# Performance work log

Measured on AMD Instinct MI355X. Metric: run time of the kernel, lower is better.

The kernel has to match this reference:

```python
import jax, jax.numpy as jnp
import numpy as np

HEAD_DIM = 64
N_HEADS = 32
N_KV_HEADS = 8
ROPE_THETA = 10000.0


def _rotate_half(x):
    h = x.shape[-1] // 2
    return jnp.concatenate([-x[..., h:], x[..., :h]], axis=-1)


def _rope_cos_sin(position_ids, head_dim, theta, dtype):
    # position_ids: [b, s] int
    inv_freq = 1.0 / (theta ** (jnp.arange(0, head_dim, 2, dtype=jnp.float32) / head_dim))
    freqs = position_ids.astype(jnp.float32)[..., None] * inv_freq  # [b, s, hd/2]
    emb = jnp.concatenate([freqs, freqs], axis=-1)                  # [b, s, hd]
    return jnp.cos(emb).astype(dtype), jnp.sin(emb).astype(dtype)


def setup_inputs() -> dict:
    key = jax.random.key(0)
    ks = jax.random.split(key, 5)
    B, S, H = 2, 2048, 2048
    KVD = N_KV_HEADS * HEAD_DIM
    x = jax.random.normal(ks[0], (B, S, H), dtype=jnp.float32)
    position_ids = jnp.broadcast_to(jnp.arange(S, dtype=jnp.int64), (B, S))
    # additive causal mask: 0 on/below diagonal, -1e9 above
    causal = jnp.triu(jnp.full((S, S), -1e9, dtype=jnp.float32), k=1)
    mask = causal[None, None, :, :]
    sc = 1.0 / np.sqrt(H)
    wq = jax.random.normal(ks[1], (H, H), dtype=jnp.float32) * sc
    wk = jax.random.normal(ks[2], (KVD, H), dtype=jnp.float32) * sc
    wv = jax.random.normal(ks[3], (KVD, H), dtype=jnp.float32) * sc
    wo = jax.random.normal(ks[4], (H, H), dtype=jnp.float32) * sc
    return {"x": x, "position_ids": position_ids, "mask": mask,
            "wq": wq, "wk": wk, "wv": wv, "wo": wo}


def reference(x, position_ids, mask, wq, wk, wv, wo):
    b, s, h = x.shape
    kv_groups = N_HEADS // N_KV_HEADS
    # projections (Linear with weight [out, in])
    xq = jnp.einsum('bsh,oh->bso', x, wq)
    xk = jnp.einsum('bsh,oh->bso', x, wk)
    xv = jnp.einsum('bsh,oh->bso', x, wv)
    q = xq.reshape(b, s, N_HEADS, HEAD_DIM).transpose(0, 2, 1, 3)      # [b,H,s,d]
    k = xk.reshape(b, s, N_KV_HEADS, HEAD_DIM).transpose(0, 2, 1, 3)   # [b,Hk,s,d]
    v = xv.reshape(b, s, N_KV_HEADS, HEAD_DIM).transpose(0, 2, 1, 3)
    cos, sin = _rope_cos_sin(position_ids, HEAD_DIM, ROPE_THETA, x.dtype)
    cos = cos[:, None, :, :]  # [b,1,s,d]
    sin = sin[:, None, :, :]
    q = q * cos + _rotate_half(q) * sin
    k = k * cos + _rotate_half(k) * sin
    # GQA expand
    k = jnp.repeat(k, kv_groups, axis=1)  # [b,H,s,d]
    v = jnp.repeat(v, kv_groups, axis=1)
    scale = 1.0 / np.sqrt(HEAD_DIM)
    attn = jnp.einsum('bhqd,bhkd->bhqk', q, k) * scale
    attn = attn + mask[:, :, :s, :s]
    attn = jax.nn.softmax(attn.astype(jnp.float32), axis=-1).astype(q.dtype)
    out = jnp.einsum('bhqk,bhkd->bhqd', attn, v)        # [b,H,s,d]
    out = out.transpose(0, 2, 1, 3).reshape(b, s, h)
    return jnp.einsum('bsh,oh->bso', out, wo)
```

## Files before the change

kernel.cpp:

```cpp
#include <hip/hip_runtime.h>

typedef __bf16 bf16;
typedef __bf16 bf16x4 __attribute__((ext_vector_type(4)));
typedef __bf16 bf16x8 __attribute__((ext_vector_type(8)));
typedef float f32x4 __attribute__((ext_vector_type(4)));

#define MFMA16(a, b, c) __builtin_amdgcn_mfma_f32_16x16x32_bf16(a, b, c, 0, 0, 0)
#define L2E 1.44269504088896340736f

__device__ inline float exp2_hw(float x) {
  float r;
  asm("v_exp_f32 %0, %1" : "=v"(r) : "v"(x));
  return r;
}

__device__ inline bf16x8 cvt8(const float* __restrict__ p) {
  float4 f0 = ((const float4*)p)[0];
  float4 f1 = ((const float4*)p)[1];
  bf16x8 v;
  v[0] = (bf16)f0.x; v[1] = (bf16)f0.y; v[2] = (bf16)f0.z; v[3] = (bf16)f0.w;
  v[4] = (bf16)f1.x; v[5] = (bf16)f1.y; v[6] = (bf16)f1.z; v[7] = (bf16)f1.w;
  return v;
}

__device__ inline void gl_lds16(const bf16* g, bf16* l) {
  __builtin_amdgcn_global_load_lds(
      (const __attribute__((address_space(1))) unsigned int*)g,
      (__attribute__((address_space(3))) unsigned int*)l, 16, 0, 0);
}

__global__ void detect_kernel(const unsigned* __restrict__ mask,
                              int* __restrict__ flag) {
  *flag = (mask[0] != 0u) ? 1 : 0;
}

__global__ __launch_bounds__(256) void convert_kernel(
    const void* __restrict__ s0, bf16* __restrict__ d0, int n0,
    const void* __restrict__ s1, bf16* __restrict__ d1, int n1,
    const void* __restrict__ s2, bf16* __restrict__ d2, int n2,
    const void* __restrict__ s3, bf16* __restrict__ d3, int n3,
    float2* __restrict__ tab, const int* __restrict__ flag) {
  const int gid = blockIdx.x * 256 + threadIdx.x;
  if (tab && gid < 65536) {
    int s = gid >> 5, fi = gid & 31;
    float inv = 1.0f / powf(10000.0f, (float)(2 * fi) / 64.0f);
    float fr = (float)s * inv;
    tab[gid] = make_float2(cosf(fr), sinf(fr));
  }
  const int isb = *flag;
  const int c0 = n0 >> 3, c1 = c0 + (n1 >> 3), c2 = c1 + (n2 >> 3);
  const int total = c2 + (n3 >> 3);
  for (int c = gid; c < total; c += gridDim.x * 256) {
    const void* s; bf16* d; int off;
    if (c < c0)      { s = s0; d = d0; off = c; }
    else if (c < c1) { s = s1; d = d1; off = c - c0; }
    else if (c < c2) { s = s2; d = d2; off = c - c1; }
    else             { s = s3; d = d3; off = c - c2; }
    if (isb) ((uint4*)d)[off] = ((const uint4*)s)[off];
    else     ((bf16x8*)d)[off] = cvt8((const float*)s + (size_t)off * 8);
  }
}

template <int MODE>
__global__ __launch_bounds__(256) void gemm_bt(
    const bf16* __restrict__ Ab, const bf16* __restrict__ Wq,
    const bf16* __restrict__ Wk, const bf16* __restrict__ Wv,
    void* __restrict__ O0, bf16* __restrict__ O1, bf16* __restrict__ O2,
    const float2* __restrict__ rtab, const int* __restrict__ flag) {
  const int K = 2048;
  __shared__ __align__(16) bf16 As[128 * 32];
  __shared__ __align__(16) bf16 Bs[64 * 32];

  const int m0 = blockIdx.x * 128;
  const int n0 = blockIdx.y * 64;

  const bf16* W;
  int nw0;
  if (MODE == 0) {
    if (n0 < 2048) { W = Wq; nw0 = n0; }
    else if (n0 < 2560) { W = Wk; nw0 = n0 - 2048; }
    else { W = Wv; nw0 = n0 - 2560; }
  } else {
    W = Wq; nw0 = n0;
  }

  const int t = threadIdx.x;
  const int w = t >> 6, lane = t & 63, quad = lane >> 4, l15 = lane & 15;

  const int ca = t, cb = t + 256;
  const int ra = ca >> 2, rb = cb >> 2;
  const bf16* ga0 = Ab + (size_t)(m0 + ra) * K + (((ca & 3) ^ ((ra >> 1) & 3)) * 8);
  const bf16* ga1 = Ab + (size_t)(m0 + rb) * K + (((cb & 3) ^ ((rb >> 1) & 3)) * 8);
  const bf16* gb0 = W + (size_t)(nw0 + ra) * K + (((ca & 3) ^ ((ra >> 1) & 3)) * 8);
  bf16* lA0 = &As[w * 512];
  bf16* lA1 = &As[2048 + w * 512];
  bf16* lB0 = &Bs[w * 512];

  f32x4 acc[2][4] = {};

  const int sa = (quad ^ ((l15 >> 1) & 3)) << 3;

  for (int k0 = 0; k0 < K; k0 += 32) {
    __syncthreads();
    gl_lds16(ga0 + k0, lA0);
    gl_lds16(ga1 + k0, lA1);
    gl_lds16(gb0 + k0, lB0);
    __syncthreads();

    bf16x8 a[2], b[4];
#pragma unroll
    for (int i = 0; i < 2; i++)
      a[i] = *(const bf16x8*)&As[(w * 32 + i * 16 + l15) * 32 + sa];
#pragma unroll
    for (int j = 0; j < 4; j++)
      b[j] = *(const bf16x8*)&Bs[(j * 16 + l15) * 32 + sa];
#pragma unroll
    for (int i = 0; i < 2; i++)
#pragma unroll
      for (int j = 0; j < 4; j++)
        acc[i][j] = MFMA16(a[i], b[j], acc[i][j]);
  }

  if (MODE == 0 && n0 >= 2560) {
#pragma unroll
    for (int i = 0; i < 2; i++)
#pragma unroll
      for (int j = 0; j < 4; j++) {
        int m = m0 + w * 32 + i * 16 + quad * 4;
        int n = (n0 - 2560) + j * 16 + l15;
        int hh = n >> 6, d = n & 63;
        int b_ = m >> 11, s = m & 2047;
        bf16x4 pv;
#pragma unroll
        for (int r = 0; r < 4; r++) pv[r] = (bf16)acc[i][j][r];
        *(bf16x4*)&O2[(((size_t)b_ * 8 + hh) * 64 + d) * 2048 + s] = pv;
      }
    return;
  }

  const int isb = *flag;

  if (MODE == 0) {
#pragma unroll
    for (int i = 0; i < 2; i++) {
      int mb = m0 + w * 32 + i * 16 + quad * 4;
#pragma unroll
      for (int r = 0; r < 4; r++) {
        int s = (mb + r) & 2047;
#pragma unroll
        for (int jp = 0; jp < 2; jp++) {
          int fi = jp * 16 + l15;
          float2 cs = rtab[s * 32 + fi];
          float cb = cs.x, sb = cs.y;
          if (isb) { cb = (float)(bf16)cb; sb = (float)(bf16)sb; }
          float v0 = acc[i][jp][r], v1 = acc[i][jp + 2][r];
          acc[i][jp][r]     = v0 * cb - v1 * sb;
          acc[i][jp + 2][r] = v1 * cb + v0 * sb;
        }
      }
    }
    const bool isQ = (n0 < 2048);
    const float qs = isQ ? 0.125f : 1.0f;
#pragma unroll
    for (int i = 0; i < 2; i++)
#pragma unroll
      for (int j = 0; j < 4; j++)
#pragma unroll
        for (int r = 0; r < 4; r++) {
          int m = m0 + w * 32 + i * 16 + quad * 4 + r;
          int b_ = m >> 11, s = m & 2047;
          bf16 bv = (bf16)(acc[i][j][r] * qs);
          if (isQ) {
            int n = n0 + j * 16 + l15;
            int h = n >> 6, d = n & 63;
            ((bf16*)O0)[(((size_t)b_ * 32 + h) * 2048 + s) * 64 + d] = bv;
          } else {
            int nn = n0 - 2048 + j * 16 + l15;
            int h = nn >> 6, d = nn & 63;
            O1[(((size_t)b_ * 8 + h) * 2048 + s) * 64 + d] = bv;
          }
        }
    return;
  }

#pragma unroll
  for (int i = 0; i < 2; i++)
#pragma unroll
    for (int j = 0; j < 4; j++)
#pragma unroll
      for (int r = 0; r < 4; r++) {
        int m = m0 + w * 32 + i * 16 + quad * 4 + r;
        int n = n0 + j * 16 + l15;
        float fv = acc[i][j][r];
        if (isb) ((bf16*)O0)[(size_t)m * 2048 + n] = (bf16)fv;
        else     ((float*)O0)[(size_t)m * 2048 + n] = fv;
      }
}

__global__ __launch_bounds__(512) void flash_kernel(
    const bf16* __restrict__ qb, const bf16* __restrict__ kb,
    const bf16* __restrict__ vb, bf16* __restrict__ ao) {
  __shared__ __align__(16) bf16 SM[8704 + 8 * 16 * 72];
  bf16* Ks = SM;
  bf16* Vt = SM + 4096;
  bf16* Ps = SM + 8704;

  const int bx = blockIdx.x;
  const int h = blockIdx.y;
  const int b = blockIdx.z;
  const int kvh = h >> 2;
  const int t = threadIdx.x, w = t >> 6, lane = t & 63;
  const int quad = lane >> 4, l15 = lane & 15;

  const bf16* kg = kb + ((size_t)b * 8 + kvh) * 2048 * 64;
  const bf16* vg = vb + ((size_t)b * 8 + kvh) * 64 * 2048;

  const int srow = t >> 3;
  const int sslot = t & 7;
  const int kofs = srow * 64 + ((sslot ^ (srow & 7)) << 3);
  const int vofs = srow * 72 + sslot * 8;
  bf16* psw = Ps + w * (16 * 72);

#pragma unroll 1
  for (int ti = 0; ti < 2; ti++) {
    const int tile = (ti == 0) ? bx : 15 - bx;
    const int q0b = tile * 128;
    const bf16* qg = qb + (((size_t)b * 32 + h) * 2048 + q0b) * 64;

    __syncthreads();
#pragma unroll
    for (int i = 0; i < 2; i++) {
      int c = t + i * 512;
      int row = c >> 3, slot = c & 7;
      *(uint4*)&SM[row * 64 + ((slot ^ (row & 7)) << 3)] = ((const uint4*)qg)[c];
    }
    uint4 kr = ((const uint4*)kg)[t];
    uint4 vr = *(const uint4*)(vg + (size_t)srow * 2048 + sslot * 8);
    __syncthreads();
    const int qrow = w * 16 + l15;
    bf16x8 aq0 = *(const bf16x8*)&SM[qrow * 64 + ((quad ^ (qrow & 7)) << 3)];
    bf16x8 aq1 = *(const bf16x8*)&SM[qrow * 64 + (((4 + quad) ^ (qrow & 7)) << 3)];

    f32x4 Oacc[4] = {};
    float m_sm = -1e30f, l_sm = 0.0f;

    const int nk = q0b + 128;
    const int qmin = q0b + w * 16;
    const int qmax = qmin + 15;
    const int qr_sm = qmin + l15;

    for (int k0 = 0; k0 < nk; k0 += 64) {
      __syncthreads();
      *(uint4*)&Ks[kofs] = kr;
      *(uint4*)&Vt[vofs] = vr;
      __syncthreads();

      if (k0 + 64 < nk) {
        kr = *((const uint4*)(kg + (size_t)(k0 + 64) * 64) + t);
        vr = *(const uint4*)(vg + (size_t)srow * 2048 + (k0 + 64) + sslot * 8);
      }

      f32x4 sf[4] = {};
#pragma unroll
      for (int sub = 0; sub < 4; sub++) {
        if (k0 + sub * 16 <= qmax) {
          int rr = sub * 16 + l15;
          bf16x8 bk0 = *(const bf16x8*)&Ks[rr * 64 + ((quad ^ (rr & 7)) << 3)];
          bf16x8 bk1 = *(const bf16x8*)&Ks[rr * 64 + (((4 + quad) ^ (rr & 7)) << 3)];
          sf[sub] = MFMA16(bk0, aq0, sf[sub]);
          sf[sub] = MFMA16(bk1, aq1, sf[sub]);
        }
      }

      if (k0 + 64 > qmin) {
#pragma unroll
        for (int sub = 0; sub < 4; sub++) {
          int kk = k0 + sub * 16 + quad * 4;
#pragma unroll
          for (int r = 0; r < 4; r++)
            if (kk + r > qr_sm) sf[sub][r] = -1e30f;
        }
      }

      float mx;
      {
        f32x4 t4;
#pragma unroll
        for (int r = 0; r < 4; r++)
          t4[r] = fmaxf(fmaxf(sf[0][r], sf[1][r]), fmaxf(sf[2][r], sf[3][r]));
        mx = fmaxf(fmaxf(t4[0], t4[1]), fmaxf(t4[2], t4[3]));
      }
      mx = fmaxf(mx, __shfl_xor(mx, 16));
      mx = fmaxf(mx, __shfl_xor(mx, 32));

      if (!__all(mx <= m_sm + 8.0f)) {
        float mnew = fmaxf(m_sm, mx);
        float alpha = exp2_hw((m_sm - mnew) * L2E);
        l_sm *= alpha;
        m_sm = mnew;
        f32x4 apv;
#pragma unroll
        for (int r = 0; r < 4; r++) apv[r] = __shfl(alpha, quad * 4 + r);
#pragma unroll
        for (int tt = 0; tt < 4; tt++)
#pragma unroll
          for (int r = 0; r < 4; r++) Oacc[tt][r] *= apv[r];
      }

      const float ml2 = m_sm * L2E;
#pragma unroll
      for (int sub = 0; sub < 4; sub++)
#pragma unroll
        for (int r = 0; r < 4; r++)
          sf[sub][r] = exp2_hw(fmaf(sf[sub][r], L2E, -ml2));

      float rs;
      {
        f32x4 t4;
#pragma unroll
        for (int r = 0; r < 4; r++)
          t4[r] = (sf[0][r] + sf[1][r]) + (sf[2][r] + sf[3][r]);
        rs = (t4[0] + t4[1]) + (t4[2] + t4[3]);
      }
      rs += __shfl_xor(rs, 16);
      rs += __shfl_xor(rs, 32);
      l_sm += rs;

#pragma unroll
      for (int sub = 0; sub < 4; sub++) {
        bf16x4 pk;
#pragma unroll
        for (int r = 0; r < 4; r++) pk[r] = (bf16)sf[sub][r];
        *(bf16x4*)&psw[l15 * 72 + sub * 16 + quad * 4] = pk;
      }
      asm volatile("s_waitcnt lgkmcnt(0)" ::: "memory");
      __builtin_amdgcn_sched_barrier(0);

      bf16x8 ap0 = *(const bf16x8*)&psw[l15 * 72 + quad * 8];
#pragma unroll
      for (int tt = 0; tt < 4; tt++) {
        bf16x8 bv = *(const bf16x8*)&Vt[(tt * 16 + l15) * 72 + quad * 8];
        Oacc[tt] = MFMA16(ap0, bv, Oacc[tt]);
      }
      if (k0 + 32 <= qmax) {
        bf16x8 ap1 = *(const bf16x8*)&psw[l15 * 72 + 32 + quad * 8];
#pragma unroll
        for (int tt = 0; tt < 4; tt++) {
          bf16x8 bv = *(const bf16x8*)&Vt[(tt * 16 + l15) * 72 + 32 + quad * 8];
          Oacc[tt] = MFMA16(ap1, bv, Oacc[tt]);
        }
      }
    }

    f32x4 lv;
#pragma unroll
    for (int r = 0; r < 4; r++) lv[r] = __shfl(l_sm, quad * 4 + r);
#pragma unroll
    for (int tt = 0; tt < 4; tt++)
#pragma unroll
      for (int r = 0; r < 4; r++) {
        int m = q0b + w * 16 + quad * 4 + r;
        ao[((size_t)b * 2048 + m) * 2048 + h * 64 + tt * 16 + l15] =
            (bf16)(Oacc[tt][r] / lv[r]);
      }
  }
}

extern "C" void kernel_launch(void* const* d_in, const int* in_sizes, int n_in,
                              void* d_out, int out_size, void* d_ws,
                              size_t ws_size, hipStream_t stream) {
  const void* x = d_in[0];
  const unsigned* maskw = (const unsigned*)d_in[2];
  const void* wq = d_in[3];
  const void* wk = d_in[4];
  const void* wv = d_in[5];
  const void* wo = d_in[6];

  char* ws = (char*)d_ws;
  bf16* qbuf  = (bf16*)(ws);
  bf16* kbuf  = (bf16*)(ws + 16777216);
  bf16* vbuf  = (bf16*)(ws + 20971520);
  bf16* wob   = (bf16*)(ws + 16777216);
  bf16* aobuf = (bf16*)(ws + 25165824);
  bf16* xb    = (bf16*)(ws + 25165824);
  int* flag   = (int*)(ws + 41943040);
  bf16* wqb   = (bf16*)(ws + 41943104);
  bf16* wkb   = (bf16*)(ws + 50331712);
  bf16* wvb   = (bf16*)(ws + 52428864);
  float2* rtab = (float2*)(ws + 54526016);

  detect_kernel<<<1, 1, 0, stream>>>(maskw, flag);
  convert_kernel<<<2048, 256, 0, stream>>>(x, xb, 8388608, wq, wqb, 4194304,
                                           wk, wkb, 1048576, wv, wvb, 1048576,
                                           rtab, flag);
  gemm_bt<0><<<dim3(32, 48), 256, 0, stream>>>(xb, wqb, wkb, wvb, qbuf, kbuf,
                                               vbuf, rtab, flag);
  flash_kernel<<<dim3(8, 32, 2), 512, 0, stream>>>(qbuf, kbuf, vbuf, aobuf);
  convert_kernel<<<2048, 256, 0, stream>>>(wo, wob, 4194304, nullptr, nullptr,
                                           0, nullptr, nullptr, 0, nullptr,
                                           nullptr, 0, nullptr, flag);
  gemm_bt<1><<<dim3(32, 32), 256, 0, stream>>>(aobuf, wob, nullptr, nullptr,
                                               d_out, nullptr, nullptr, rtab,
                                               flag);
}
```

Measured before the change: 340.4 us.

## Double-buffer LDS tiles in projection GEMM to overlap loads with MFMA

Splits the shared-memory A and B tiles into two buffers and prefetches the next K-slice via direct global-to-LDS loads while computing on the current one. Manual vmcnt/lgkmcnt waits and raw s_barrier replace the pair of __syncthreads per iteration. The goal is to hide global memory latency behind the matrix-core work. It doubles LDS use per block, which may reduce occupancy, and the hand-written wait counts rely on the exact number of outstanding loads being correct.

Result: no change. 338.8 us (-0.5%).

```diff
diff --git a/kernel.cpp b/kernel.cpp
--- a/kernel.cpp
+++ b/kernel.cpp
@@ -68,8 +68,8 @@
     void* __restrict__ O0, bf16* __restrict__ O1, bf16* __restrict__ O2,
     const float2* __restrict__ rtab, const int* __restrict__ flag) {
   const int K = 2048;
-  __shared__ __align__(16) bf16 As[128 * 32];
-  __shared__ __align__(16) bf16 Bs[64 * 32];
+  __shared__ __align__(16) bf16 As[2][128 * 32];
+  __shared__ __align__(16) bf16 Bs[2][64 * 32];
 
   const int m0 = blockIdx.x * 128;
   const int n0 = blockIdx.y * 64;
@@ -92,33 +92,46 @@
   const bf16* ga0 = Ab + (size_t)(m0 + ra) * K + (((ca & 3) ^ ((ra >> 1) & 3)) * 8);
   const bf16* ga1 = Ab + (size_t)(m0 + rb) * K + (((cb & 3) ^ ((rb >> 1) & 3)) * 8);
   const bf16* gb0 = W + (size_t)(nw0 + ra) * K + (((ca & 3) ^ ((ra >> 1) & 3)) * 8);
-  bf16* lA0 = &As[w * 512];
-  bf16* lA1 = &As[2048 + w * 512];
-  bf16* lB0 = &Bs[w * 512];
 
   f32x4 acc[2][4] = {};
 
   const int sa = (quad ^ ((l15 >> 1) & 3)) << 3;
 
-  for (int k0 = 0; k0 < K; k0 += 32) {
-    __syncthreads();
-    gl_lds16(ga0 + k0, lA0);
-    gl_lds16(ga1 + k0, lA1);
-    gl_lds16(gb0 + k0, lB0);
-    __syncthreads();
+  const int NT = K / 32;
+  gl_lds16(ga0, &As[0][w * 512]);
+  gl_lds16(ga1, &As[0][2048 + w * 512]);
+  gl_lds16(gb0, &Bs[0][w * 512]);
+
+#pragma unroll 2
+  for (int ti = 0; ti < NT; ti++) {
+    const int cur = ti & 1;
+    const int k0 = ti * 32;
+    if (ti + 1 < NT) {
+      const int nxt = cur ^ 1;
+      gl_lds16(ga0 + k0 + 32, &As[nxt][w * 512]);
+      gl_lds16(ga1 + k0 + 32, &As[nxt][2048 + w * 512]);
+      gl_lds16(gb0 + k0 + 32, &Bs[nxt][w * 512]);
+      asm volatile("s_waitcnt vmcnt(3)" ::: "memory");
+    } else {
+      asm volatile("s_waitcnt vmcnt(0)" ::: "memory");
+    }
+    __builtin_amdgcn_s_barrier();
 
     bf16x8 a[2], b[4];
 #pragma unroll
     for (int i = 0; i < 2; i++)
-      a[i] = *(const bf16x8*)&As[(w * 32 + i * 16 + l15) * 32 + sa];
+      a[i] = *(const bf16x8*)&As[cur][(w * 32 + i * 16 + l15) * 32 + sa];
 #pragma unroll
     for (int j = 0; j < 4; j++)
-      b[j] = *(const bf16x8*)&Bs[(j * 16 + l15) * 32 + sa];
+      b[j] = *(const bf16x8*)&Bs[cur][(j * 16 + l15) * 32 + sa];
 #pragma unroll
     for (int i = 0; i < 2; i++)
 #pragma unroll
       for (int j = 0; j < 4; j++)
         acc[i][j] = MFMA16(a[i], b[j], acc[i][j]);
+
+    asm volatile("s_waitcnt lgkmcnt(0)" ::: "memory");
+    __builtin_amdgcn_s_barrier();
   }
 
   if (MODE == 0 && n0 >= 2560) {
```
